# Optimization experiments

Measured on AMD Instinct MI355X. Metric: run time of the kernel, lower is better.

## Reference

```python
import jax, jax.numpy as jnp
import numpy as np

N_NODES = 100000
N_PAIRS = 800000  # undirected pairs; E = 2*N_PAIRS directed edges
D_FEAT = 128
THRESHOLD = 0.01
EPS = 1e-8


def setup_inputs() -> dict:
    key = jax.random.key(0)
    k1, k2, k3, k4 = jax.random.split(key, 4)
    # symmetric edge list without self-loops (each undirected pair in both directions)
    src = jax.random.randint(k1, (N_PAIRS,), 0, N_NODES)
    off = jax.random.randint(k2, (N_PAIRS,), 1, N_NODES)
    dst = (src + off) % N_NODES  # guaranteed != src
    edge_index = jnp.stack([jnp.concatenate([src, dst]),
                            jnp.concatenate([dst, src])]).astype(jnp.int64)
    w_half = jax.random.uniform(k3, (N_PAIRS,), dtype=jnp.float32)
    edge_weight = jnp.concatenate([w_half, w_half])
    features = jax.random.normal(k4, (N_NODES, D_FEAT), dtype=jnp.float32)
    return {"edge_index": edge_index, "edge_weight": edge_weight, "features": features}


def reference(edge_index, edge_weight, features):
    # Cosine-similarity edge dropping (Jaccard.forward, non-binary feature path).
    # Original: build NxN sparse adj, take triu, per-edge cosine sim, zero edges
    # with sim < threshold, symmetrize (triu + triu^T), read back at edge positions.
    # For a symmetric duplicate-free edge list this equals per-edge masking, with
    # diagonal entries doubled by triu + triu^T.
    src, dst = edge_index[0], edge_index[1]
    node_norm = jnp.sqrt(jnp.sum(features * features, axis=-1))  # [N]
    inner = jnp.sum(features[src] * features[dst], axis=-1)       # [E] per-edge gather+dot
    sim = inner / (node_norm[src] * node_norm[dst] + EPS)
    keep = (sim >= THRESHOLD).astype(edge_weight.dtype)
    diag_double = 1.0 + (src == dst).astype(edge_weight.dtype)    # triu+triu^T doubles diagonal
    return edge_weight * keep * diag_double
```

## Files before the change

### kernel.cpp

```cpp
#include <hip/hip_runtime.h>
#include <hip/hip_fp16.h>

#define D_FEAT 128
#define THRESH 0.01f
#define EPS_F  1e-8f

#define NPB 64
#define ROWF 132

typedef _Float16 half2_t __attribute__((ext_vector_type(2)));


__device__ float edge_out_scalar(const float* __restrict__ feat,
                                 float w, int s, int d) {
#pragma clang fp contract(off)
    const float* fs = feat + (size_t)s * D_FEAT;
    const float* fd = feat + (size_t)d * D_FEAT;
    float r[8], rs[8], rd[8];
#pragma unroll
    for (int j = 0; j < 8; ++j) {
        float a = fs[j], b = fd[j];
        r[j]  = a * b;
        rs[j] = a * a;
        rd[j] = b * b;
    }
    for (int k = 1; k < 16; ++k) {
#pragma unroll
        for (int j = 0; j < 8; ++j) {
            float a = fs[8 * k + j], b = fd[8 * k + j];
            r[j]  = r[j]  + a * b;
            rs[j] = rs[j] + a * a;
            rd[j] = rd[j] + b * b;
        }
    }
    float inner = ((r[0]  + r[1])  + (r[2]  + r[3]))  + ((r[4]  + r[5])  + (r[6]  + r[7]));
    float ss    = ((rs[0] + rs[1]) + (rs[2] + rs[3])) + ((rs[4] + rs[5]) + (rs[6] + rs[7]));
    float dd    = ((rd[0] + rd[1]) + (rd[2] + rd[3])) + ((rd[4] + rd[5]) + (rd[6] + rd[7]));
    float ns = __fsqrt_rn(ss);
    float nd = __fsqrt_rn(dd);
    float denom = ns * nd + EPS_F;
    float sim = inner / denom;
    float keep = (sim >= THRESH) ? 1.0f : 0.0f;
    float diag = (s == d) ? 2.0f : 1.0f;
    return (w * keep) * diag;
}

__device__ __forceinline__ float exact_sim_pairlanes(const float* __restrict__ feat,
                                                     int src, int dst, int h) {
#pragma clang fp contract(off)
    const float4* fs = (const float4*)(feat + (size_t)src * D_FEAT);
    const float4* fd = (const float4*)(feat + (size_t)dst * D_FEAT);
    float r[4], rs[4], rd[4];
    {
        float4 a = fs[h];
        float4 b = fd[h];
        r[0]  = a.x * b.x; r[1]  = a.y * b.y; r[2]  = a.z * b.z; r[3]  = a.w * b.w;
        rs[0] = a.x * a.x; rs[1] = a.y * a.y; rs[2] = a.z * a.z; rs[3] = a.w * a.w;
        rd[0] = b.x * b.x; rd[1] = b.y * b.y; rd[2] = b.z * b.z; rd[3] = b.w * b.w;
    }
#pragma unroll
    for (int k = 1; k < 16; ++k) {
        float4 a = fs[2 * k + h];
        float4 b = fd[2 * k + h];
        r[0]  = r[0]  + a.x * b.x;  r[1]  = r[1]  + a.y * b.y;
        r[2]  = r[2]  + a.z * b.z;  r[3]  = r[3]  + a.w * b.w;
        rs[0] = rs[0] + a.x * a.x;  rs[1] = rs[1] + a.y * a.y;
        rs[2] = rs[2] + a.z * a.z;  rs[3] = rs[3] + a.w * a.w;
        rd[0] = rd[0] + b.x * b.x;  rd[1] = rd[1] + b.y * b.y;
        rd[2] = rd[2] + b.z * b.z;  rd[3] = rd[3] + b.w * b.w;
    }
    float A  = (r[0]  + r[1])  + (r[2]  + r[3]);
    float As = (rs[0] + rs[1]) + (rs[2] + rs[3]);
    float Ad = (rd[0] + rd[1]) + (rd[2] + rd[3]);

    float inner = A  + __shfl_xor(A, 1, 64);
    float ssE   = As + __shfl_xor(As, 1, 64);
    float ddE   = Ad + __shfl_xor(Ad, 1, 64);

    float ns    = __fsqrt_rn(ssE);
    float nd    = __fsqrt_rn(ddE);
    float den   = ns * nd + EPS_F;
    return inner / den;
}

__device__ __forceinline__ float exact_inner_pairlanes(const float* __restrict__ feat,
                                                       int src, int dst, int h) {
#pragma clang fp contract(off)
    const float4* fs = (const float4*)(feat + (size_t)src * D_FEAT);
    const float4* fd = (const float4*)(feat + (size_t)dst * D_FEAT);
    float r[4];
    {
        float4 a = fs[h];
        float4 b = fd[h];
        r[0] = a.x * b.x; r[1] = a.y * b.y; r[2] = a.z * b.z; r[3] = a.w * b.w;
    }
#pragma unroll
    for (int k = 1; k < 16; ++k) {
        float4 a = fs[2 * k + h];
        float4 b = fd[2 * k + h];
        r[0] = r[0] + a.x * b.x;  r[1] = r[1] + a.y * b.y;
        r[2] = r[2] + a.z * b.z;  r[3] = r[3] + a.w * b.w;
    }
    float A = (r[0] + r[1]) + (r[2] + r[3]);
    return A + __shfl_xor(A, 1, 64);
}

__global__ __launch_bounds__(256) void jaccard_edge_kernel(
    const int* __restrict__ ei, const float* __restrict__ w,
    const float* __restrict__ feat, float* __restrict__ out,
    int P, int E)
{
    int t    = blockIdx.x * blockDim.x + threadIdx.x;
    int pair = t >> 1;
    int half = t & 1;
    if (pair >= P) return;

    int src = ei[pair];
    int dst = ei[E + pair];

    float sim  = exact_sim_pairlanes(feat, src, dst, half);
    float keep = (sim >= THRESH) ? 1.0f : 0.0f;

    if (half == 0) {
        float diag = (src == dst) ? 2.0f : 1.0f;
        out[pair] = (w[pair] * keep) * diag;
        int m = P + pair;
        if (m < E) {
            int s2 = ei[m];
            int d2 = ei[E + m];
            if (s2 == dst && d2 == src) out[m] = (w[m] * keep) * diag;
            else                        out[m] = edge_out_scalar(feat, w[m], s2, d2);
        }
    }
}

__global__ __launch_bounds__(256) void norm_convert_kernel(
    const float* __restrict__ feat, __half* __restrict__ hfeat,
    float* __restrict__ nrm, int nNodes)
{
#pragma clang fp contract(off)
    __shared__ float lds[NPB * ROWF];
    __shared__ float lr[NPB];

    int block0 = blockIdx.x * NPB;
    int nvalid = nNodes - block0; if (nvalid > NPB) nvalid = NPB;
    int tid = threadIdx.x;

    const float4* gsrc = (const float4*)(feat + (size_t)block0 * D_FEAT);
    float4* lds4 = (float4*)lds;
    int nf4 = nvalid * (D_FEAT / 4);
    for (int i = tid; i < nf4; i += 256) {
        int n = i >> 5, c = i & 31;
        lds4[n * (ROWF / 4) + c] = gsrc[i];
    }
    __syncthreads();

    int ln = tid >> 2, q = tid & 3;
    if (ln < nvalid) {
        const float2* lrow = (const float2*)(lds + ln * ROWF);
        float2 a = lrow[q];
        float r0 = a.x * a.x, r1 = a.y * a.y;
#pragma unroll
        for (int k = 1; k < 16; ++k) {
            float2 v = lrow[4 * k + q];
            r0 = r0 + v.x * v.x;
            r1 = r1 + v.y * v.y;
        }
        float s  = r0 + r1;
        float ss = s + __shfl_xor(s, 1, 64);
        ss       = ss + __shfl_xor(ss, 2, 64);
        float na = __fsqrt_rn(ss);
        if (q == 0) {
            nrm[block0 + ln] = na;
            bool ok = isfinite(na) && (na >= 0.03f);
            lr[ln] = ok ? (1.0f / na) : __builtin_nanf("");
        }
    }
    __syncthreads();

    uint4* gdst = (uint4*)(hfeat + (size_t)block0 * D_FEAT);
    int nu4 = nvalid * (D_FEAT / 8);
    for (int i = tid; i < nu4; i += 256) {
        int n = i >> 4, c = i & 15;
        float r = lr[n];
        const float4* lp = (const float4*)(lds + n * ROWF + 8 * c);
        float4 x = lp[0], y = lp[1];
        __half2 h0 = __floats2half2_rn(x.x * r, x.y * r);
        __half2 h1 = __floats2half2_rn(x.z * r, x.w * r);
        __half2 h2 = __floats2half2_rn(y.x * r, y.y * r);
        __half2 h3 = __floats2half2_rn(y.z * r, y.w * r);
        uint4 o;
        o.x = __builtin_bit_cast(unsigned, h0);
        o.y = __builtin_bit_cast(unsigned, h1);
        o.z = __builtin_bit_cast(unsigned, h2);
        o.w = __builtin_bit_cast(unsigned, h3);
        gdst[i] = o;
    }
}

__device__ __forceinline__ float dot8_f16(uint4 ua, uint4 ub, float acc) {
    acc = __builtin_amdgcn_fdot2(__builtin_bit_cast(half2_t, ua.x),
                                 __builtin_bit_cast(half2_t, ub.x), acc, false);
    acc = __builtin_amdgcn_fdot2(__builtin_bit_cast(half2_t, ua.y),
                                 __builtin_bit_cast(half2_t, ub.y), acc, false);
    acc = __builtin_amdgcn_fdot2(__builtin_bit_cast(half2_t, ua.z),
                                 __builtin_bit_cast(half2_t, ub.z), acc, false);
    acc = __builtin_amdgcn_fdot2(__builtin_bit_cast(half2_t, ua.w),
                                 __builtin_bit_cast(half2_t, ub.w), acc, false);
    return acc;
}

__global__ __launch_bounds__(256) void jaccard_edge_f16u_kernel(
    const int* __restrict__ ei, const float* __restrict__ w,
    const float* __restrict__ feat, const __half* __restrict__ hfeat,
    const float* __restrict__ nrm, float* __restrict__ out, int P, int E)
{
#pragma clang fp contract(off)
    int t    = blockIdx.x * blockDim.x + threadIdx.x;
    int pair = t >> 2;
    int q    = t & 3;
    if (pair >= P) return;

    int src = __builtin_nontemporal_load(ei + pair);
    int dst = __builtin_nontemporal_load(ei + E + pair);

    float wp  = __builtin_nontemporal_load(w + pair);
    int   m   = P + pair;
    bool  hasm = (m < E);
    int s2 = 0, d2 = 0;
    float wm = 0.f;
    if (hasm) {
        s2 = __builtin_nontemporal_load(ei + m);
        d2 = __builtin_nontemporal_load(ei + E + m);
        wm = __builtin_nontemporal_load(w + m);
    }

    const uint4* ha = (const uint4*)(hfeat + (size_t)src * D_FEAT);
    const uint4* hb = (const uint4*)(hfeat + (size_t)dst * D_FEAT);

    uint4 A[4], B[4];
#pragma unroll
    for (int k = 0; k < 4; ++k) {
        A[k] = ha[4 * k + q];
        B[k] = hb[4 * k + q];
    }

    float d = 0.f;
#pragma unroll
    for (int k = 0; k < 4; ++k) d = dot8_f16(A[k], B[k], d);

    d += __shfl_xor(d, 1, 64);
    float dot = d + __shfl_xor(d, 2, 64);

    float diff = dot - THRESH;
    const float bnd = 1.2e-3f;

    float keep;
    if (fabsf(diff) > bnd && fabsf(dot) < 2.0f) {
        keep = (diff >= 0.f) ? 1.0f : 0.0f;
    } else {
        float se = 0.f;
        if (q < 2) {
            float inner = exact_inner_pairlanes(feat, src, dst, q);
            float den   = nrm[src] * nrm[dst] + EPS_F;
            se = inner / den;
        }
        keep = (se >= THRESH) ? 1.0f : 0.0f;
    }

    if (q == 0) {
        float diag = (src == dst) ? 2.0f : 1.0f;
        __builtin_nontemporal_store((wp * keep) * diag, out + pair);
        if (hasm) {
            if (s2 == dst && d2 == src) {
                __builtin_nontemporal_store((wm * keep) * diag, out + m);
            } else {
                out[m] = edge_out_scalar(feat, wm, s2, d2);
            }
        }
    }
}

extern "C" void kernel_launch(void* const* d_in, const int* in_sizes, int n_in,
                              void* d_out, int out_size, void* d_ws, size_t ws_size,
                              hipStream_t stream) {
    const int*   ei   = (const int*)d_in[0];
    const float* w    = (const float*)d_in[1];
    const float* feat = (const float*)d_in[2];
    float*       out  = (float*)d_out;

    int E = in_sizes[1];
    int P = E - E / 2;
    long nfeat = in_sizes[2];
    long nNodes = nfeat / D_FEAT;
    size_t need = (size_t)nfeat * sizeof(__half) + (size_t)nNodes * sizeof(float);

    if (ws_size < need || (nfeat % D_FEAT) != 0) {
        int threads = 2 * P;
        int grid = (threads + 255) / 256;
        jaccard_edge_kernel<<<grid, 256, 0, stream>>>(ei, w, feat, out, P, E);
        return;
    }

    __half* hfeat = (__half*)d_ws;
    float*  nrm   = (float*)((char*)d_ws + (size_t)nfeat * sizeof(__half));

    int gridA = (int)((nNodes + NPB - 1) / NPB);
    norm_convert_kernel<<<gridA, 256, 0, stream>>>(feat, hfeat, nrm, (int)nNodes);

    int tB = 4 * P;
    jaccard_edge_f16u_kernel<<<(tB + 255) / 256, 256, 0, stream>>>(
        ei, w, feat, hfeat, nrm, out, P, E);
}
```

Before: 152.9 us.

## Bin edges by source slice and destination block to improve gather locality

Adds a counting-sort pipeline (clear, histogram, scan, scatter) that groups edges into 2048 buckets keyed by source-node slice and destination-node block. The per-edge FP16 dot kernel then walks the records slice by slice, so feature rows in the L2/MALL cache get reused instead of fetched at random. The cost is four extra launches, atomics, and writing and re-reading about 20 bytes per edge of record arrays.

```diff
diff --git a/kernel.cpp b/kernel.cpp
--- a/kernel.cpp
+++ b/kernel.cpp
@@ -7,6 +7,8 @@
 
 #define NPB 64
 #define ROWF 132
+
+#define NBUCK 2048
 
 typedef _Float16 half2_t __attribute__((ext_vector_type(2)));
 
@@ -281,6 +283,174 @@
     }
 }
 
+__device__ __forceinline__ int bucket_key(int a, int b, int nN) {
+    int s   = (int)(((long long)a * 8)   / nN); if (s > 7)     s = 7;     if (s < 0)   s = 0;
+    int blk = (int)(((long long)b * 256) / nN); if (blk > 255) blk = 255; if (blk < 0) blk = 0;
+    return (s << 8) | blk;
+}
+
+__global__ __launch_bounds__(256) void bin_clear_kernel(int* __restrict__ cnt) {
+    int t = threadIdx.x;
+    for (int i = t; i < NBUCK; i += 256) cnt[i] = 0;
+}
+
+__global__ __launch_bounds__(256) void bin_hist_kernel(
+    const int* __restrict__ ei, int* __restrict__ cnt,
+    int P, int E, int nN)
+{
+    int stride = gridDim.x * blockDim.x;
+    for (int p = blockIdx.x * blockDim.x + threadIdx.x; p < P; p += stride) {
+        int src = ei[p];
+        int dst = ei[E + p];
+        atomicAdd(cnt + bucket_key(src, dst, nN), 1);
+        int m = P + p;
+        if (m < E) {
+            int s2 = ei[m];
+            int d2 = ei[E + m];
+            if (!(s2 == dst && d2 == src))
+                atomicAdd(cnt + bucket_key(s2, d2, nN), 1);
+        }
+    }
+}
+
+__global__ __launch_bounds__(256) void bin_scan_kernel(
+    const int* __restrict__ cnt, int* __restrict__ cursor, int* __restrict__ meta)
+{
+    __shared__ int part[256];
+    int tid = threadIdx.x;
+    int c[8];
+    int sum = 0;
+#pragma unroll
+    for (int i = 0; i < 8; ++i) { c[i] = cnt[8 * tid + i]; sum += c[i]; }
+    part[tid] = sum;
+    __syncthreads();
+    for (int off = 1; off < 256; off <<= 1) {
+        int v = (tid >= off) ? part[tid - off] : 0;
+        __syncthreads();
+        part[tid] += v;
+        __syncthreads();
+    }
+    int excl = part[tid] - sum;
+    int run = excl;
+#pragma unroll
+    for (int i = 0; i < 8; ++i) { cursor[8 * tid + i] = run; run += c[i]; }
+    if ((tid & 31) == 0) {
+        int s = tid >> 5;
+        meta[s] = excl;
+        if (s > 0) meta[8 + s - 1] = excl;
+    }
+    if (tid == 255) meta[8 + 7] = part[255];
+}
+
+__global__ __launch_bounds__(256) void bin_scatter_kernel(
+    const int* __restrict__ ei, const float* __restrict__ w,
+    int* __restrict__ cursor,
+    int* __restrict__ rsrc, int* __restrict__ rdst,
+    float* __restrict__ rwp, float* __restrict__ rwm,
+    unsigned* __restrict__ ridx,
+    int P, int E, int nN)
+{
+    int stride = gridDim.x * blockDim.x;
+    for (int p = blockIdx.x * blockDim.x + threadIdx.x; p < P; p += stride) {
+        int src = ei[p];
+        int dst = ei[E + p];
+        float wp = w[p];
+        int m = P + p;
+        bool mm = false;
+        int s2 = 0, d2 = 0;
+        float wm = 0.f;
+        if (m < E) {
+            s2 = ei[m];
+            d2 = ei[E + m];
+            wm = w[m];
+            mm = (s2 == dst && d2 == src);
+        }
+        int pos = atomicAdd(cursor + bucket_key(src, dst, nN), 1);
+        rsrc[pos] = src;
+        rdst[pos] = dst;
+        rwp[pos]  = wp;
+        rwm[pos]  = mm ? wm : 0.f;
+        ridx[pos] = (unsigned)p | (mm ? 0x80000000u : 0u);
+        if (m < E && !mm) {
+            int pos2 = atomicAdd(cursor + bucket_key(s2, d2, nN), 1);
+            rsrc[pos2] = s2;
+            rdst[pos2] = d2;
+            rwp[pos2]  = wm;
+            rwm[pos2]  = 0.f;
+            ridx[pos2] = (unsigned)m;
+        }
+    }
+}
+
+__global__ __launch_bounds__(256) void jaccard_binned_kernel(
+    const int* __restrict__ rsrc, const int* __restrict__ rdst,
+    const float* __restrict__ rwp, const float* __restrict__ rwm,
+    const unsigned* __restrict__ ridx, const int* __restrict__ meta,
+    const float* __restrict__ feat, const __half* __restrict__ hfeat,
+    const float* __restrict__ nrm, float* __restrict__ out, int P)
+{
+#pragma clang fp contract(off)
+    int slice = blockIdx.x & 7;
+    int s0 = meta[slice];
+    int s1 = meta[8 + slice];
+    int quad = threadIdx.x >> 2;
+    int q    = threadIdx.x & 3;
+    int blocksPerSlice = gridDim.x >> 3;
+    int bchunk = blockIdx.x >> 3;
+
+    for (int start = s0 + bchunk * 64; start < s1; start += blocksPerSlice * 64) {
+        int rec  = start + quad;
+        bool act = (rec < s1);
+        int recc = act ? rec : (s1 - 1);
+
+        int src      = rsrc[recc];
+        int dst      = rdst[recc];
+        float wp     = rwp[recc];
+        float wm     = rwm[recc];
+        unsigned ide = ridx[recc];
+
+        const uint4* ha = (const uint4*)(hfeat + (size_t)src * D_FEAT);
+        const uint4* hb = (const uint4*)(hfeat + (size_t)dst * D_FEAT);
+
+        uint4 A[4], B[4];
+#pragma unroll
+        for (int k = 0; k < 4; ++k) {
+            A[k] = ha[4 * k + q];
+            B[k] = hb[4 * k + q];
+        }
+
+        float d = 0.f;
+#pragma unroll
+        for (int k = 0; k < 4; ++k) d = dot8_f16(A[k], B[k], d);
+
+        d += __shfl_xor(d, 1, 64);
+        float dot = d + __shfl_xor(d, 2, 64);
+
+        float diff = dot - THRESH;
+        const float bnd = 1.2e-3f;
+
+        float keep;
+        if (fabsf(diff) > bnd && fabsf(dot) < 2.0f) {
+            keep = (diff >= 0.f) ? 1.0f : 0.0f;
+        } else {
+            float se = 0.f;
+            if (q < 2) {
+                float inner = exact_inner_pairlanes(feat, src, dst, q);
+                float den   = nrm[src] * nrm[dst] + EPS_F;
+                se = inner / den;
+            }
+            keep = (se >= THRESH) ? 1.0f : 0.0f;
+        }
+
+        if (act && q == 0) {
+            int idx = (int)(ide & 0x7fffffffu);
+            float diag = (src == dst) ? 2.0f : 1.0f;
+            out[idx] = (wp * keep) * diag;
+            if (ide & 0x80000000u) out[idx + P] = (wm * keep) * diag;
+        }
+    }
+}
+
 extern "C" void kernel_launch(void* const* d_in, const int* in_sizes, int n_in,
                               void* d_out, int out_size, void* d_ws, size_t ws_size,
                               hipStream_t stream) {
@@ -293,22 +463,56 @@
     int P = E - E / 2;
     long nfeat = in_sizes[2];
     long nNodes = nfeat / D_FEAT;
-    size_t need = (size_t)nfeat * sizeof(__half) + (size_t)nNodes * sizeof(float);
-
-    if (ws_size < need || (nfeat % D_FEAT) != 0) {
+
+    size_t hbytes  = (size_t)nfeat * sizeof(__half);
+    size_t need1   = hbytes + (size_t)nNodes * sizeof(float);
+
+    if (P <= 0) return;
+
+    if (ws_size < need1 || (nfeat % D_FEAT) != 0) {
         int threads = 2 * P;
         int grid = (threads + 255) / 256;
         jaccard_edge_kernel<<<grid, 256, 0, stream>>>(ei, w, feat, out, P, E);
         return;
     }
 
-    __half* hfeat = (__half*)d_ws;
-    float*  nrm   = (float*)((char*)d_ws + (size_t)nfeat * sizeof(__half));
+    size_t o = 0;
+    __half* hfeat = (__half*)((char*)d_ws + o);  o += hbytes;
+    o = (o + 255) & ~(size_t)255;
+    float* nrm = (float*)((char*)d_ws + o);      o += (size_t)nNodes * sizeof(float);
+    o = (o + 255) & ~(size_t)255;
+    size_t orec = o;
+    int*      rsrc = (int*)((char*)d_ws + o);       o += (size_t)E * 4;
+    int*      rdst = (int*)((char*)d_ws + o);       o += (size_t)E * 4;
+    float*    rwp  = (float*)((char*)d_ws + o);     o += (size_t)E * 4;
+    float*    rwm  = (float*)((char*)d_ws + o);     o += (size_t)E * 4;
+    unsigned* ridx = (unsigned*)((char*)d_ws + o);  o += (size_t)E * 4;
+    int* cnt    = (int*)((char*)d_ws + o);          o += NBUCK * 4;
+    int* cursor = (int*)((char*)d_ws + o);          o += NBUCK * 4;
+    int* meta   = (int*)((char*)d_ws + o);          o += 32 * 4;
+    size_t need2 = o;
 
     int gridA = (int)((nNodes + NPB - 1) / NPB);
     norm_convert_kernel<<<gridA, 256, 0, stream>>>(feat, hfeat, nrm, (int)nNodes);
 
-    int tB = 4 * P;
-    jaccard_edge_f16u_kernel<<<(tB + 255) / 256, 256, 0, stream>>>(
-        ei, w, feat, hfeat, nrm, out, P, E);
-}
+    if (ws_size < need2 || nNodes < 8) {
+        int tB = 4 * P;
+        jaccard_edge_f16u_kernel<<<(tB + 255) / 256, 256, 0, stream>>>(
+            ei, w, feat, hfeat, nrm, out, P, E);
+        return;
+    }
+
+    int gridH = (P + 255) / 256; if (gridH > 2048) gridH = 2048;
+    bin_clear_kernel<<<1, 256, 0, stream>>>(cnt);
+    bin_hist_kernel<<<gridH, 256, 0, stream>>>(ei, cnt, P, E, (int)nNodes);
+    bin_scan_kernel<<<1, 256, 0, stream>>>(cnt, cursor, meta);
+    bin_scatter_kernel<<<gridH, 256, 0, stream>>>(ei, w, cursor,
+                                                  rsrc, rdst, rwp, rwm, ridx,
+                                                  P, E, (int)nNodes);
+
+    int bps = (P / 8 + 63) / 64 + 2;
+    int gridB = 8 * bps;
+    jaccard_binned_kernel<<<gridB, 256, 0, stream>>>(
+        rsrc, rdst, rwp, rwm, ridx, meta, feat, hfeat, nrm, out, P);
+    (void)orec;
+}
```

After: 363.3 us. 138% more time.
